# Kernel optimization log

Hardware: AMD Instinct MI355X
Metric: run time of the kernel (lower is better)

The kernel has to match this reference:

```python
import jax, jax.numpy as jnp
import numpy as np

SCALING = 16.0  # lora_alpha
R = 16


def setup_inputs() -> dict:
    key = jax.random.key(0)
    ks = jax.random.split(key, 6)
    B, S, D_IN, D_OUT = 4, 2048, 4096, 4096
    x = jax.random.normal(ks[0], (B, S, D_IN), dtype=jnp.float32)
    W = jax.random.normal(ks[1], (D_OUT, D_IN), dtype=jnp.float32) * 0.02
    b = jax.random.normal(ks[2], (D_OUT,), dtype=jnp.float32) * 0.02
    lora_A = jax.random.normal(ks[3], (R, D_IN), dtype=jnp.float32) * 0.02
    lora_B = jax.random.normal(ks[4], (D_OUT, R), dtype=jnp.float32) * 0.02
    lora_c = jax.random.uniform(ks[5], (R, 1), dtype=jnp.float32)
    return {"x": x, "W": W, "b": b, "lora_A": lora_A, "lora_B": lora_B, "lora_c": lora_c}


def reference(x, W, b, lora_A, lora_B, lora_c):
    # Base (quantized-in-torch, dense here) linear: x @ W.T + b
    result = jnp.einsum("bsi,oi->bso", x, W) + b
    # LoRA correction: x @ (A * c).T @ B.T * scaling / r
    # Contract down to rank-r first to avoid a [D_IN, D_OUT] intermediate.
    A_scaled = lora_A * lora_c                       # [r, D_IN]
    h = jnp.einsum("bsi,ri->bsr", x, A_scaled)       # [B, S, r] (small)
    lora_out = jnp.einsum("bsr,or->bso", h, lora_B) * (SCALING / R)
    return result + lora_out
```

## Files before the change

### kernel.cpp

```cpp
#include <hip/hip_runtime.h>
#include <hip/hip_bf16.h>
#include <stdint.h>
#include <stddef.h>

#define D_IN   4096
#define D_OUT  4096
#define M_TOT  8192
#define R_RANK 16
#define LORA_SCALE 1.0f

typedef __attribute__((ext_vector_type(8))) short short8;
typedef __attribute__((ext_vector_type(4))) short short4v;
typedef __attribute__((ext_vector_type(16))) float f32x16;

#define GL2LDS16(g, l)                                                  \
  __builtin_amdgcn_global_load_lds(                                     \
      (const __attribute__((address_space(1))) void*)(g),               \
      (__attribute__((address_space(3))) void*)(l), 16, 0, 0)

#define PACK_BLOCKS 16384
#define PREP_BLOCKS 4096

__global__ __launch_bounds__(256) void pack_prep(
    const float* __restrict__ x, __hip_bfloat16* __restrict__ Xp,
    const float* __restrict__ W, const float* __restrict__ A,
    const float* __restrict__ c, const float* __restrict__ B,
    __hip_bfloat16* __restrict__ Wp) {
  if (blockIdx.x < PACK_BLOCKS) {
    size_t idx = ((size_t)blockIdx.x * 256 + threadIdx.x) * 8;
    float4 v0 = *(const float4*)(x + idx);
    float4 v1 = *(const float4*)(x + idx + 4);
    __hip_bfloat16 t[8];
    t[0] = __float2bfloat16(v0.x); t[1] = __float2bfloat16(v0.y);
    t[2] = __float2bfloat16(v0.z); t[3] = __float2bfloat16(v0.w);
    t[4] = __float2bfloat16(v1.x); t[5] = __float2bfloat16(v1.y);
    t[6] = __float2bfloat16(v1.z); t[7] = __float2bfloat16(v1.w);
    *(short8*)(Xp + idx) = *(const short8*)t;
    return;
  }
  int bid = blockIdx.x - PACK_BLOCKS;
  int t  = threadIdx.x;
  int i  = (bid & 3) * 1024 + t * 4;
  int o0 = (bid >> 2) * 4;

  float4 a4[R_RANK];
#pragma unroll
  for (int r = 0; r < R_RANK; r++) {
    float4 v = *(const float4*)(A + r * D_IN + i);
    float cr = c[r] * LORA_SCALE;
    v.x *= cr; v.y *= cr; v.z *= cr; v.w *= cr;
    a4[r] = v;
  }
#pragma unroll
  for (int oo = 0; oo < 4; oo++) {
    int o = o0 + oo;
    float4 w = *(const float4*)(W + (size_t)o * D_IN + i);
#pragma unroll
    for (int r = 0; r < R_RANK; r++) {
      float br = B[o * R_RANK + r];
      w.x += br * a4[r].x; w.y += br * a4[r].y;
      w.z += br * a4[r].z; w.w += br * a4[r].w;
    }
    __hip_bfloat16 tb[4];
    tb[0] = __float2bfloat16(w.x); tb[1] = __float2bfloat16(w.y);
    tb[2] = __float2bfloat16(w.z); tb[3] = __float2bfloat16(w.w);
    *(short4v*)(Wp + (size_t)o * D_IN + i) = *(const short4v*)tb;
  }
}

#define BK 64
#define NT (D_IN / BK)

#define SOFF(BUFI, AB, KH) ((((BUFI) * 2 + (AB)) * 2 + (KH)) * 8192)

#define VMCNT(N) asm volatile("s_waitcnt vmcnt(" #N ")" ::: "memory")
#define HARD_BARRIER() asm volatile("s_barrier" ::: "memory")
#define SOFT_BARRIER() __builtin_amdgcn_s_barrier()

#define STAGE_HALF(BUFI, AB, KH, TS)                                         \
  do {                                                                       \
    const __hip_bfloat16* _src = (AB) ? Wp : Xp;                             \
    const int _rb = (AB) ? n0 : m0;                                          \
    const int _kb = (TS) * BK + (KH) * 32;                                   \
    _Pragma("unroll")                                                        \
    for (int _is = 0; _is < 2; ++_is) {                                      \
      const int _p = _is * 512 + tid;                     \
      const int _row = _p >> 2;                                              \
      const int _c = (_p & 3) ^ ((_row >> 1) & 3);      \
      GL2LDS16(_src + (size_t)(_rb + _row) * D_IN + _kb + _c * 8,            \
               smem + SOFF(BUFI, AB, KH) + _p * 8);                          \
    }                                                                        \
  } while (0)

#define LOAD_AF(BUFI, H, RH)                                                 \
  _Pragma("unroll")                                                          \
  for (int _i = 0; _i < 4; ++_i)                                             \
    af[_i] = *(const short8*)(smem + SOFF(BUFI, 0, H) +                      \
                              (wm * 128 + ((RH) * 2 + (_i & 1)) * 32 + l31)  \
                                  * 32 +                                     \
                              (((_i >> 1) * 2 + lh) ^ xr) * 8);

#define LOAD_BF(BUFI, H)                                                     \
  _Pragma("unroll")                                                          \
  for (int _i = 0; _i < 4; ++_i)                                             \
    bf[_i] = *(const short8*)(smem + SOFF(BUFI, 1, H) +                      \
                              (wn * 64 + (_i & 1) * 32 + l31) * 32 +         \
                              (((_i >> 1) * 2 + lh) ^ xr) * 8);

#define MFMA_QUAD(RH)                                                        \
  do {                                                                       \
    __builtin_amdgcn_s_setprio(1);                                           \
    _Pragma("unroll")                                                        \
    for (int _kfh = 0; _kfh < 2; ++_kfh)                                     \
      _Pragma("unroll")                                                      \
      for (int _r = 0; _r < 2; ++_r)                                         \
        _Pragma("unroll")                                                    \
        for (int _n = 0; _n < 2; ++_n)                                       \
          acc[(RH) * 2 + _r][_n] = __builtin_amdgcn_mfma_f32_32x32x16_bf16(  \
              af[_kfh * 2 + _r], bf[_kfh * 2 + _n],                          \
              acc[(RH) * 2 + _r][_n], 0, 0, 0);                              \
    __builtin_amdgcn_s_setprio(0);                                           \
  } while (0)

#define TILE_BODY(BUFI, NBUF, T, DO_STAGE)                                   \
  do {                                                                       \
                                                  \
    LOAD_AF(BUFI, 0, 0);                                                     \
    LOAD_BF(BUFI, 0);                                                        \
    if (DO_STAGE) STAGE_HALF(NBUF, 0, 0, (T) + 1);                           \
    SOFT_BARRIER();                                                          \
    MFMA_QUAD(0);                                                            \
    SOFT_BARRIER();                                                          \
                                                  \
    LOAD_AF(BUFI, 0, 1);                                                     \
    if (DO_STAGE) STAGE_HALF(NBUF, 1, 0, (T) + 1);                           \
    SOFT_BARRIER();                                                          \
    MFMA_QUAD(1);                                                            \
    if (DO_STAGE) { VMCNT(4); } else { VMCNT(0); }                           \
    HARD_BARRIER();                                                          \
                                                  \
    LOAD_AF(BUFI, 1, 0);                                                     \
    LOAD_BF(BUFI, 1);                                                        \
    if (DO_STAGE) STAGE_HALF(NBUF, 0, 1, (T) + 1);                           \
    SOFT_BARRIER();                                                          \
    MFMA_QUAD(0);                                                            \
    SOFT_BARRIER();                                                          \
                                                  \
    LOAD_AF(BUFI, 1, 1);                                                     \
    if (DO_STAGE) STAGE_HALF(NBUF, 1, 1, (T) + 1);                           \
    SOFT_BARRIER();                                                          \
    MFMA_QUAD(1);                                                            \
    if (DO_STAGE) { VMCNT(4); } else { VMCNT(0); }                           \
    HARD_BARRIER();                                                          \
  } while (0)

__global__ __launch_bounds__(512, 2) void gemm_256(
    const __hip_bfloat16* __restrict__ Xp,
    const __hip_bfloat16* __restrict__ Wp,
    const float* __restrict__ bias,
    float* __restrict__ out) {
  __shared__ __align__(16) __hip_bfloat16 smem[2 * 2 * 2 * 8192];

  const int tid  = threadIdx.x;
  const int wid  = tid >> 6;
  const int lane = tid & 63;
  const int wm = wid >> 2;
  const int wn = wid & 3;
  const int l31 = lane & 31;
  const int lh  = lane >> 5;
  const int xr  = (l31 >> 1) & 3;
  const int m0 = blockIdx.y * 256;
  const int n0 = blockIdx.x * 256;

  f32x16 acc[4][2];
#pragma unroll
  for (int i = 0; i < 4; i++)
#pragma unroll
    for (int j = 0; j < 2; j++)
#pragma unroll
      for (int k = 0; k < 16; k++) acc[i][j][k] = 0.f;

  short8 af[4];
  short8 bf[4];

  STAGE_HALF(0, 0, 0, 0);
  STAGE_HALF(0, 1, 0, 0);
  STAGE_HALF(0, 0, 1, 0);
  STAGE_HALF(0, 1, 1, 0);
  VMCNT(4);
  HARD_BARRIER();

#pragma unroll 1
  for (int t = 0; t < NT - 2; t += 2) {
    TILE_BODY(0, 1, t, 1);
    TILE_BODY(1, 0, t + 1, 1);
  }
  TILE_BODY(0, 1, NT - 2, 1);
  TILE_BODY(1, 0, NT - 1, 0);

  float bv[2];
#pragma unroll
  for (int nb = 0; nb < 2; ++nb) bv[nb] = bias[n0 + wn * 64 + nb * 32 + l31];
#pragma unroll
  for (int rb = 0; rb < 4; ++rb) {
#pragma unroll
    for (int r = 0; r < 16; ++r) {
      const int row = m0 + wm * 128 + rb * 32 + (r & 3) + 8 * (r >> 2) + 4 * lh;
      float* po = out + (size_t)row * D_OUT + n0 + wn * 64 + l31;
      po[0]  = acc[rb][0][r] + bv[0];
      po[32] = acc[rb][1][r] + bv[1];
    }
  }
}

extern "C" void kernel_launch(void* const* d_in, const int* in_sizes, int n_in,
                              void* d_out, int out_size, void* d_ws, size_t ws_size,
                              hipStream_t stream) {
  const float* x  = (const float*)d_in[0];
  const float* W  = (const float*)d_in[1];
  const float* b  = (const float*)d_in[2];
  const float* lA = (const float*)d_in[3];
  const float* lB = (const float*)d_in[4];
  const float* lc = (const float*)d_in[5];
  float* out = (float*)d_out;

  char* ws = (char*)d_ws;
  __hip_bfloat16* Xp = (__hip_bfloat16*)ws;
  __hip_bfloat16* Wp = (__hip_bfloat16*)(ws + (size_t)67108864);

  pack_prep<<<dim3(PACK_BLOCKS + PREP_BLOCKS), dim3(256), 0, stream>>>(
      x, Xp, W, lA, lc, lB, Wp);
  gemm_256<<<dim3(D_OUT / 256, M_TOT / 256), dim3(512), 0, stream>>>(Xp, Wp, b, out);
}
```

Baseline: 524.2 us.

## Store full 64-wide K rows in LDS with 8-way XOR swizzle and staggered staging

The LDS tiles move from two 32-element K halves to single 64-element rows. Each row is now fetched as one contiguous 128-byte segment by 8 lanes, with an 8-way XOR swizzle on the 16-byte chunks to avoid bank conflicts. Global-to-LDS staging is reordered by row groups: B first, then the A row blocks each MFMA quad needs, and the vmcnt waits are placed so each quad waits only for its own rows. The goal is better coalescing and less waiting on loads, at the cost of a more fragile wait-count ordering.

```diff
diff --git a/kernel.cpp b/kernel.cpp
--- a/kernel.cpp
+++ b/kernel.cpp
@@ -71,41 +71,37 @@
 #define BK 64
 #define NT (D_IN / BK)
 
-#define SOFF(BUFI, AB, KH) ((((BUFI) * 2 + (AB)) * 2 + (KH)) * 8192)
+#define SOFF(BUFI, AB) (((BUFI) * 2 + (AB)) * 16384)
 
 #define VMCNT(N) asm volatile("s_waitcnt vmcnt(" #N ")" ::: "memory")
 #define HARD_BARRIER() asm volatile("s_barrier" ::: "memory")
 #define SOFT_BARRIER() __builtin_amdgcn_s_barrier()
 
-#define STAGE_HALF(BUFI, AB, KH, TS)                                         \
+#define STAGE_ISSUE(BUFI, AB, ISS, TS)                                       \
   do {                                                                       \
     const __hip_bfloat16* _src = (AB) ? Wp : Xp;                             \
     const int _rb = (AB) ? n0 : m0;                                          \
-    const int _kb = (TS) * BK + (KH) * 32;                                   \
-    _Pragma("unroll")                                                        \
-    for (int _is = 0; _is < 2; ++_is) {                                      \
-      const int _p = _is * 512 + tid;                     \
-      const int _row = _p >> 2;                                              \
-      const int _c = (_p & 3) ^ ((_row >> 1) & 3);      \
-      GL2LDS16(_src + (size_t)(_rb + _row) * D_IN + _kb + _c * 8,            \
-               smem + SOFF(BUFI, AB, KH) + _p * 8);                          \
-    }                                                                        \
+    const int _rl = tid >> 3;                    \
+    const int _cc = (tid & 7) ^ (_rl & 7);                                   \
+    GL2LDS16(_src + (size_t)(_rb + (ISS) * 64 + _rl) * D_IN + (TS) * BK +    \
+                 _cc * 8,                                                    \
+             smem + SOFF(BUFI, AB) + (ISS) * 4096 + tid * 8);                \
   } while (0)
 
 #define LOAD_AF(BUFI, H, RH)                                                 \
   _Pragma("unroll")                                                          \
   for (int _i = 0; _i < 4; ++_i)                                             \
-    af[_i] = *(const short8*)(smem + SOFF(BUFI, 0, H) +                      \
+    af[_i] = *(const short8*)(smem + SOFF(BUFI, 0) +                         \
                               (wm * 128 + ((RH) * 2 + (_i & 1)) * 32 + l31)  \
-                                  * 32 +                                     \
-                              (((_i >> 1) * 2 + lh) ^ xr) * 8);
+                                  * 64 +                                     \
+                              (((H) * 4 + (_i >> 1) * 2 + lh) ^ x7) * 8);
 
 #define LOAD_BF(BUFI, H)                                                     \
   _Pragma("unroll")                                                          \
   for (int _i = 0; _i < 4; ++_i)                                             \
-    bf[_i] = *(const short8*)(smem + SOFF(BUFI, 1, H) +                      \
-                              (wn * 64 + (_i & 1) * 32 + l31) * 32 +         \
-                              (((_i >> 1) * 2 + lh) ^ xr) * 8);
+    bf[_i] = *(const short8*)(smem + SOFF(BUFI, 1) +                         \
+                              (wn * 64 + (_i & 1) * 32 + l31) * 64 +         \
+                              (((H) * 4 + (_i >> 1) * 2 + lh) ^ x7) * 8);
 
 #define MFMA_QUAD(RH)                                                        \
   do {                                                                       \
@@ -124,33 +120,45 @@
 
 #define TILE_BODY(BUFI, NBUF, T, DO_STAGE)                                   \
   do {                                                                       \
-                                                  \
+                                     \
     LOAD_AF(BUFI, 0, 0);                                                     \
     LOAD_BF(BUFI, 0);                                                        \
-    if (DO_STAGE) STAGE_HALF(NBUF, 0, 0, (T) + 1);                           \
+    if (DO_STAGE) {                                                          \
+      STAGE_ISSUE(NBUF, 1, 0, (T) + 1);                                      \
+      STAGE_ISSUE(NBUF, 1, 1, (T) + 1);                                      \
+    }                                                                        \
     SOFT_BARRIER();                                                          \
     MFMA_QUAD(0);                                                            \
-    SOFT_BARRIER();                                                          \
-                                                  \
+    if (DO_STAGE) { VMCNT(2); } else { VMCNT(0); }                           \
+    HARD_BARRIER();                                                          \
+                                     \
     LOAD_AF(BUFI, 0, 1);                                                     \
-    if (DO_STAGE) STAGE_HALF(NBUF, 1, 0, (T) + 1);                           \
+    if (DO_STAGE) {                                                          \
+      STAGE_ISSUE(NBUF, 1, 2, (T) + 1);                                      \
+      STAGE_ISSUE(NBUF, 1, 3, (T) + 1);                                      \
+    }                                                                        \
     SOFT_BARRIER();                                                          \
     MFMA_QUAD(1);                                                            \
-    if (DO_STAGE) { VMCNT(4); } else { VMCNT(0); }                           \
-    HARD_BARRIER();                                                          \
-                                                  \
+    SOFT_BARRIER();                                                          \
+                                     \
     LOAD_AF(BUFI, 1, 0);                                                     \
     LOAD_BF(BUFI, 1);                                                        \
-    if (DO_STAGE) STAGE_HALF(NBUF, 0, 1, (T) + 1);                           \
+    if (DO_STAGE) {                                                          \
+      STAGE_ISSUE(NBUF, 0, 0, (T) + 1);                                      \
+      STAGE_ISSUE(NBUF, 0, 2, (T) + 1);                                      \
+    }                                                                        \
     SOFT_BARRIER();                                                          \
     MFMA_QUAD(0);                                                            \
     SOFT_BARRIER();                                                          \
-                                                  \
+      \
     LOAD_AF(BUFI, 1, 1);                                                     \
-    if (DO_STAGE) STAGE_HALF(NBUF, 1, 1, (T) + 1);                           \
+    if (DO_STAGE) {                                                          \
+      STAGE_ISSUE(NBUF, 0, 1, (T) + 1);                                      \
+      STAGE_ISSUE(NBUF, 0, 3, (T) + 1);                                      \
+    }                                                                        \
     SOFT_BARRIER();                                                          \
     MFMA_QUAD(1);                                                            \
-    if (DO_STAGE) { VMCNT(4); } else { VMCNT(0); }                           \
+    if (DO_STAGE) { VMCNT(2); } else { VMCNT(0); }                           \
     HARD_BARRIER();                                                          \
   } while (0)
 
@@ -159,7 +167,7 @@
     const __hip_bfloat16* __restrict__ Wp,
     const float* __restrict__ bias,
     float* __restrict__ out) {
-  __shared__ __align__(16) __hip_bfloat16 smem[2 * 2 * 2 * 8192];
+  __shared__ __align__(16) __hip_bfloat16 smem[2 * 2 * 16384];
 
   const int tid  = threadIdx.x;
   const int wid  = tid >> 6;
@@ -168,7 +176,7 @@
   const int wn = wid & 3;
   const int l31 = lane & 31;
   const int lh  = lane >> 5;
-  const int xr  = (l31 >> 1) & 3;
+  const int x7  = l31 & 7;
   const int m0 = blockIdx.y * 256;
   const int n0 = blockIdx.x * 256;
 
@@ -183,11 +191,15 @@
   short8 af[4];
   short8 bf[4];
 
-  STAGE_HALF(0, 0, 0, 0);
-  STAGE_HALF(0, 1, 0, 0);
-  STAGE_HALF(0, 0, 1, 0);
-  STAGE_HALF(0, 1, 1, 0);
-  VMCNT(4);
+  STAGE_ISSUE(0, 1, 0, 0);
+  STAGE_ISSUE(0, 1, 1, 0);
+  STAGE_ISSUE(0, 1, 2, 0);
+  STAGE_ISSUE(0, 1, 3, 0);
+  STAGE_ISSUE(0, 0, 0, 0);
+  STAGE_ISSUE(0, 0, 2, 0);
+  STAGE_ISSUE(0, 0, 1, 0);
+  STAGE_ISSUE(0, 0, 3, 0);
+  VMCNT(2);
   HARD_BARRIER();
 
 #pragma unroll 1
```

Measured after the change: 531.6 us. About the same (+1.4%).
